# Kernel optimization log

Measured on AMD Instinct MI355X. Metric: run time of the kernel, lower is better.

## Reference

```python
import jax, jax.numpy as jnp
import numpy as np

# Dims fixed by ExpertC.__init__ defaults
INPUT_DIM, HIDDEN, OUT_DIM, NLAYERS = 1024, 256, 256, 2
D_STATE, EXPAND, HEADDIM = 32, 2, 32
D_INNER = EXPAND * HIDDEN                      # 512
NHEADS = D_INNER // HEADDIM                    # 16
CONV_DIM = D_INNER + 2 * D_STATE               # 576 (x, B, C; ngroups=1)
D_IN_PROJ = 2 * D_INNER + 2 * D_STATE + NHEADS # 1104 (z, xBC, dt)
KCONV = 4
B, L = 16, 2048
EPS = 1e-5


def setup_inputs() -> dict:
    key = jax.random.key(0)
    ks = iter(jax.random.split(key, 40))
    rn = lambda shape, s: jax.random.normal(next(ks), shape, jnp.float32) * s
    inp = {}
    inp["x"] = rn((B, L, INPUT_DIM), 1.0)
    inp["ip_w"] = rn((INPUT_DIM, HIDDEN), INPUT_DIM ** -0.5)
    inp["ip_b"] = jnp.zeros((HIDDEN,), jnp.float32)
    inp["m_inw"] = rn((NLAYERS, HIDDEN, D_IN_PROJ), HIDDEN ** -0.5)
    inp["m_inb"] = jnp.zeros((NLAYERS, D_IN_PROJ), jnp.float32)
    inp["m_convw"] = rn((NLAYERS, CONV_DIM, KCONV), 0.3)
    inp["m_convb"] = jnp.zeros((NLAYERS, CONV_DIM), jnp.float32)
    inp["m_dtb"] = rn((NLAYERS, NHEADS), 0.5)
    inp["m_Alog"] = jnp.log(1.0 + 15.0 * jax.random.uniform(next(ks), (NLAYERS, NHEADS), jnp.float32))
    inp["m_D"] = jnp.ones((NLAYERS, NHEADS), jnp.float32)
    inp["m_nw"] = jnp.ones((NLAYERS, D_INNER), jnp.float32)
    inp["m_outw"] = rn((NLAYERS, D_INNER, HIDDEN), D_INNER ** -0.5)
    inp["m_outb"] = jnp.zeros((NLAYERS, HIDDEN), jnp.float32)
    inp["rms_w"] = jnp.ones((NLAYERS, HIDDEN), jnp.float32)
    inp["ln1_w"] = jnp.ones((HIDDEN,), jnp.float32)
    inp["ln1_b"] = jnp.zeros((HIDDEN,), jnp.float32)
    inp["w1"] = rn((HIDDEN, 2 * HIDDEN), HIDDEN ** -0.5)
    inp["b1"] = jnp.zeros((2 * HIDDEN,), jnp.float32)
    inp["w2"] = rn((2 * HIDDEN, OUT_DIM), (2 * HIDDEN) ** -0.5)
    inp["b2"] = jnp.zeros((OUT_DIM,), jnp.float32)
    inp["ln2_w"] = jnp.ones((OUT_DIM,), jnp.float32)
    inp["ln2_b"] = jnp.zeros((OUT_DIM,), jnp.float32)
    return inp


def rmsnorm(x, w):
    return x * jax.lax.rsqrt(jnp.mean(x * x, axis=-1, keepdims=True) + EPS) * w


def layernorm(x, w, b):
    m = jnp.mean(x, axis=-1, keepdims=True)
    v = jnp.mean((x - m) ** 2, axis=-1, keepdims=True)
    return (x - m) * jax.lax.rsqrt(v + EPS) * w + b


def mamba_layer(x, inw, inb, convw, convb, dtb, Alog, D, nw, outw, outb):
    b, l, _ = x.shape
    zxbcdt = x @ inw + inb                                   # (b,l,1104)
    z, xBC, dt = jnp.split(zxbcdt, [D_INNER, D_INNER + CONV_DIM], axis=-1)
    dt = jax.nn.softplus(dt + dtb)                           # (b,l,h)
    # causal depthwise conv1d (kernel 4) + silu
    xp = jnp.pad(xBC, ((0, 0), (KCONV - 1, 0), (0, 0)))
    xBC = sum(xp[:, i:i + l, :] * convw[:, i] for i in range(KCONV)) + convb
    xBC = jax.nn.silu(xBC)
    xs, Bm, Cm = jnp.split(xBC, [D_INNER, D_INNER + D_STATE], axis=-1)
    xh = xs.reshape(b, l, NHEADS, HEADDIM)                   # (b,l,h,p)
    A = -jnp.exp(Alog)                                       # (h,)
    dA = jnp.exp(dt * A)                                     # (b,l,h)
    dtx = dt[..., None] * xh                                 # (b,l,h,p)

    def step(h, inp):
        dA_t, dtx_t, B_t, C_t = inp
        # h: (b,h,p,n)
        h = h * dA_t[:, :, None, None] + dtx_t[..., None] * B_t[:, None, None, :]
        y = jnp.einsum('bhpn,bn->bhp', h, C_t)
        return h, y

    h0 = jnp.zeros((b, NHEADS, HEADDIM, D_STATE), x.dtype)
    xs_t = (jnp.moveaxis(dA, 1, 0), jnp.moveaxis(dtx, 1, 0),
            jnp.moveaxis(Bm, 1, 0), jnp.moveaxis(Cm, 1, 0))
    _, ys = jax.lax.scan(step, h0, xs_t)                     # (l,b,h,p)
    y = jnp.moveaxis(ys, 0, 1) + D[None, None, :, None] * xh
    y = y.reshape(b, l, D_INNER)
    y = rmsnorm(y * jax.nn.silu(z), nw)                      # gated RMSNorm
    return y @ outw + outb


def _expert(x, ip_w, ip_b, m_inw, m_inb, m_convw, m_convb, m_dtb, m_Alog, m_D,
            m_nw, m_outw, m_outb, rms_w, ln1_w, ln1_b, w1, b1, w2, b2, ln2_w, ln2_b):
    if x.ndim == 2:
        x = x[:, None, :]
    x = x @ ip_w + ip_b
    for i in range(NLAYERS):
        res = x
        x = mamba_layer(x, m_inw[i], m_inb[i], m_convw[i], m_convb[i], m_dtb[i],
                        m_Alog[i], m_D[i], m_nw[i], m_outw[i], m_outb[i])
        x = rmsnorm(x + res, rms_w[i])
    x = layernorm(x, ln1_w, ln1_b)
    x = jax.nn.gelu(x @ w1 + b1, approximate=False)          # dropout is eval no-op
    x = x @ w2 + b2
    return layernorm(x, ln2_w, ln2_b)


def reference(x, ip_w, ip_b, m_inw, m_inb, m_convw, m_convb, m_dtb, m_Alog, m_D,
              m_nw, m_outw, m_outb, rms_w, ln1_w, ln1_b, w1, b1, w2, b2, ln2_w, ln2_b):
    return _expert(x, ip_w, ip_b, m_inw, m_inb, m_convw, m_convb, m_dtb, m_Alog, m_D,
                   m_nw, m_outw, m_outb, rms_w, ln1_w, ln1_b, w1, b1, w2, b2, ln2_w, ln2_b)
```

## Files before the change

### kernel.cpp

```cpp
#include <hip/hip_runtime.h>

typedef __bf16 bf16;
typedef __bf16 bf16x8 __attribute__((ext_vector_type(8)));
typedef float  f32x4  __attribute__((ext_vector_type(4)));

#define EPSF 1e-5f

__device__ __forceinline__ float bf2f(bf16 x) { return (float)x; }
__device__ __forceinline__ bf16  f2bf(float x) { return (bf16)x; }
__device__ __forceinline__ float siluf(float x) { return x / (1.f + expf(-x)); }

struct PrepackArgs {
    const float* W[7];
    bf16* TH[7];
    bf16* TL[7];
    int K[7];
    int N[7];
};

__global__ __launch_bounds__(256) void prepack_kernel(PrepackArgs a)
{
    int s = blockIdx.y;
    int idx = blockIdx.x * 256 + threadIdx.x;
    int K = a.K[s], N = a.N[s];
    if (idx >= K * N) return;
    int k = idx / N, n = idx - k * N;
    float v = a.W[s][idx];
    bf16 hi = f2bf(v);
    a.TH[s][(size_t)n * K + k] = hi;
    a.TL[s][(size_t)n * K + k] = f2bf(v - bf2f(hi));
}

__global__ __launch_bounds__(256) void gemm_hl(
    const bf16* __restrict__ AH, const bf16* __restrict__ AL,
    const float* __restrict__ Af, int lda,
    const bf16* __restrict__ WTh, const bf16* __restrict__ WTl,
    const float* __restrict__ bias,
    int N, int K,
    float* __restrict__ outF, int ldF,
    bf16* __restrict__ outB, int ldB,
    bf16* __restrict__ outH, bf16* __restrict__ outL, int ldH,
    int doGelu,
    const float* __restrict__ dtb, const float* __restrict__ Alog,
    float* __restrict__ dtf, float* __restrict__ dAf)
{
    __shared__ bf16 As [128][40];
    __shared__ bf16 Als[128][40];

    const int tid  = threadIdx.x;
    const int lane = tid & 63;
    const int wid  = tid >> 6;
    const int waveM = wid & 1, waveN = wid >> 1;
    const int m16 = lane & 15, quad = lane >> 4;
    const int row0 = blockIdx.x * 128;
    const int n0   = blockIdx.y * 64;

    f32x4 acc[4][2];
#pragma unroll
    for (int i = 0; i < 4; ++i)
#pragma unroll
        for (int j = 0; j < 2; ++j)
            acc[i][j] = (f32x4){0.f, 0.f, 0.f, 0.f};

    const int ar = tid >> 1, akc = (tid & 1) * 16;

    const int bn0 = min(n0 + waveN * 32 + m16,      N - 1);
    const int bn1 = min(n0 + waveN * 32 + 16 + m16, N - 1);
    const bf16* bH0p = WTh + (size_t)bn0 * K + quad * 8;
    const bf16* bH1p = WTh + (size_t)bn1 * K + quad * 8;
    const bf16* bL0p = WTl + (size_t)bn0 * K + quad * 8;
    const bf16* bL1p = WTl + (size_t)bn1 * K + quad * 8;

    bf16x8 bH[2], bL[2], bHn[2], bLn[2];
    bH[0] = *(const bf16x8*)(bH0p);
    bH[1] = *(const bf16x8*)(bH1p);
    bL[0] = *(const bf16x8*)(bL0p);
    bL[1] = *(const bf16x8*)(bL1p);

    for (int k0 = 0; k0 < K; k0 += 32) {
        if (AH) {
            const bf16* s0 = AH + (size_t)(row0 + ar) * lda + k0 + akc;
            const bf16* s1 = AL + (size_t)(row0 + ar) * lda + k0 + akc;
            *(uint4*)&As [ar][akc]     = *(const uint4*)s0;
            *(uint4*)&As [ar][akc + 8] = *(const uint4*)(s0 + 8);
            *(uint4*)&Als[ar][akc]     = *(const uint4*)s1;
            *(uint4*)&Als[ar][akc + 8] = *(const uint4*)(s1 + 8);
        } else {
            const float* asrc = Af + (size_t)(row0 + ar) * lda + k0 + akc;
            bf16* dh = &As [ar][akc];
            bf16* dl = &Als[ar][akc];
#pragma unroll
            for (int c = 0; c < 4; ++c) {
                float4 f = ((const float4*)asrc)[c];
#pragma unroll
                for (int e = 0; e < 4; ++e) {
                    float v = (&f.x)[e];
                    bf16 hi = f2bf(v);
                    dh[c * 4 + e] = hi;
                    dl[c * 4 + e] = f2bf(v - bf2f(hi));
                }
            }
        }
        __syncthreads();

        const bool more = (k0 + 32) < K;
        if (more) {
            int kn = k0 + 32;
            bHn[0] = *(const bf16x8*)(bH0p + kn);
            bHn[1] = *(const bf16x8*)(bH1p + kn);
            bLn[0] = *(const bf16x8*)(bL0p + kn);
            bLn[1] = *(const bf16x8*)(bL1p + kn);
        }

        bf16x8 aH[4], aL[4];
#pragma unroll
        for (int mi = 0; mi < 4; ++mi) {
            aH[mi] = *(const bf16x8*)&As [waveM * 64 + mi * 16 + m16][quad * 8];
            aL[mi] = *(const bf16x8*)&Als[waveM * 64 + mi * 16 + m16][quad * 8];
        }

#pragma unroll
        for (int mi = 0; mi < 4; ++mi)
#pragma unroll
            for (int ni = 0; ni < 2; ++ni) {
                acc[mi][ni] = __builtin_amdgcn_mfma_f32_16x16x32_bf16(
                    aH[mi], bH[ni], acc[mi][ni], 0, 0, 0);
                acc[mi][ni] = __builtin_amdgcn_mfma_f32_16x16x32_bf16(
                    aH[mi], bL[ni], acc[mi][ni], 0, 0, 0);
                acc[mi][ni] = __builtin_amdgcn_mfma_f32_16x16x32_bf16(
                    aL[mi], bH[ni], acc[mi][ni], 0, 0, 0);
            }
        __syncthreads();

        if (more) {
            bH[0] = bHn[0]; bH[1] = bHn[1];
            bL[0] = bLn[0]; bL[1] = bLn[1];
        }
    }

#pragma unroll
    for (int ni = 0; ni < 2; ++ni) {
        int col = n0 + waveN * 32 + ni * 16 + m16;
        if (col >= N) continue;
        float bv = bias ? bias[col] : 0.f;
#pragma unroll
        for (int mi = 0; mi < 4; ++mi) {
#pragma unroll
            for (int r = 0; r < 4; ++r) {
                int row = row0 + waveM * 64 + mi * 16 + quad * 4 + r;
                float v = acc[mi][ni][r] + bv;
                if (dtf && col >= 1088) {
                    int head = col - 1088;
                    float xx = v + dtb[head];
                    float sp = (xx > 20.f) ? xx : log1pf(expf(xx));
                    float A  = -expf(Alog[head]);
                    dtf[(size_t)row * 16 + head] = sp;
                    dAf[(size_t)row * 16 + head] = expf(sp * A);
                } else {
                    if (doGelu) v = 0.5f * v * (1.f + erff(v * 0.70710678118654752f));
                    if (outB) outB[(size_t)row * ldB + col] = f2bf(v);
                    if (outF) outF[(size_t)row * ldF + col] = v;
                    if (outH) {
                        bf16 hi = f2bf(v);
                        outH[(size_t)row * ldH + col] = hi;
                        outL[(size_t)row * ldH + col] = f2bf(v - bf2f(hi));
                    }
                }
            }
        }
    }
}

__global__ __launch_bounds__(192) void conv_kernel(
    const bf16* __restrict__ zx,
    const float* __restrict__ cw,
    const float* __restrict__ cb,
    float* __restrict__ xs,
    float* __restrict__ Bc,
    float* __restrict__ Cc)
{
    int row = blockIdx.x;
    int ch  = blockIdx.y * 192 + threadIdx.x;
    int l   = row & 2047;
    float acc = cb[ch];
#pragma unroll
    for (int i = 0; i < 4; ++i) {
        int ls = l + i - 3;
        if (ls >= 0)
            acc += bf2f(zx[(size_t)(row + i - 3) * 1104 + 512 + ch]) * cw[ch * 4 + i];
    }
    float s = siluf(acc);
    if (ch < 512)      xs[(size_t)row * 512 + ch]        = s;
    else if (ch < 544) Bc[(size_t)row * 32 + (ch - 512)] = s;
    else               Cc[(size_t)row * 32 + (ch - 544)] = s;
}

#define QCH   256
#define NCH   8

struct StepB  { float Bv[16]; float da, dtv, xv; };
struct StepBC { float Bv[16]; float Cv[16]; float da, dtv, xv; };

__device__ __forceinline__ void load_stepB(
    StepB& S, const float* Bc, const float* dtf, const float* dAf,
    const float* xs, size_t r, int h, int p, int nb)
{
    const float4* bp = (const float4*)(Bc + r * 32 + nb);
    *(float4*)&S.Bv[0]  = bp[0];
    *(float4*)&S.Bv[4]  = bp[1];
    *(float4*)&S.Bv[8]  = bp[2];
    *(float4*)&S.Bv[12] = bp[3];
    S.da  = dAf[r * 16 + h];
    S.dtv = dtf[r * 16 + h];
    S.xv  = xs[r * 512 + h * 32 + p];
}

__device__ __forceinline__ void load_stepBC(
    StepBC& S, const float* Bc, const float* Cc, const float* dtf,
    const float* dAf, const float* xs, size_t r, int h, int p, int nb)
{
    const float4* bp = (const float4*)(Bc + r * 32 + nb);
    *(float4*)&S.Bv[0]  = bp[0];
    *(float4*)&S.Bv[4]  = bp[1];
    *(float4*)&S.Bv[8]  = bp[2];
    *(float4*)&S.Bv[12] = bp[3];
    const float4* cp = (const float4*)(Cc + r * 32 + nb);
    *(float4*)&S.Cv[0]  = cp[0];
    *(float4*)&S.Cv[4]  = cp[1];
    *(float4*)&S.Cv[8]  = cp[2];
    *(float4*)&S.Cv[12] = cp[3];
    S.da  = dAf[r * 16 + h];
    S.dtv = dtf[r * 16 + h];
    S.xv  = xs[r * 512 + h * 32 + p];
}

__global__ __launch_bounds__(64) void scan_phase1(
    const float* __restrict__ xs,
    const float* __restrict__ Bc,
    const float* __restrict__ dtf,
    const float* __restrict__ dAf,
    float* __restrict__ cs,
    float* __restrict__ cp)
{
    int blk = blockIdx.x;
    int bh = blk >> 3, c = blk & (NCH - 1);
    int b = bh >> 4, h = bh & 15;
    int lane = threadIdx.x;
    int p = lane & 31, half = lane >> 5, nb = half * 16;
    float hs[16];
#pragma unroll
    for (int j = 0; j < 16; ++j) hs[j] = 0.f;
    float P = 1.f;
    size_t rb = (size_t)b * 2048 + (size_t)c * QCH;

    StepB S0, S1;
    load_stepB(S0, Bc, dtf, dAf, xs, rb, h, p, nb);

    for (int t = 0; t < QCH; t += 2) {
        load_stepB(S1, Bc, dtf, dAf, xs, rb + t + 1, h, p, nb);
        {
            float dtx = S0.dtv * S0.xv, da = S0.da;
#pragma unroll
            for (int j = 0; j < 16; ++j)
                hs[j] = fmaf(hs[j], da, dtx * S0.Bv[j]);
            P *= da;
        }
        if (t + 2 < QCH)
            load_stepB(S0, Bc, dtf, dAf, xs, rb + t + 2, h, p, nb);
        {
            float dtx = S1.dtv * S1.xv, da = S1.da;
#pragma unroll
            for (int j = 0; j < 16; ++j)
                hs[j] = fmaf(hs[j], da, dtx * S1.Bv[j]);
            P *= da;
        }
    }

    float* dst = cs + (size_t)blk * 1024 + lane * 16;
#pragma unroll
    for (int q = 0; q < 4; ++q)
        ((float4*)dst)[q] = (float4){hs[q*4], hs[q*4+1], hs[q*4+2], hs[q*4+3]};
    if (lane == 0) cp[blk] = P;
}

__global__ __launch_bounds__(64) void scan_phase2(
    float* __restrict__ cs,
    const float* __restrict__ cp)
{
    int bh = blockIdx.x;
    int lane = threadIdx.x;
    float H[16];
#pragma unroll
    for (int j = 0; j < 16; ++j) H[j] = 0.f;
    for (int c = 0; c < NCH; ++c) {
        float* base = cs + ((size_t)(bh * NCH + c)) * 1024 + lane * 16;
        float E[16];
#pragma unroll
        for (int q = 0; q < 4; ++q) {
            float4 v = ((const float4*)base)[q];
            E[q*4] = v.x; E[q*4+1] = v.y; E[q*4+2] = v.z; E[q*4+3] = v.w;
        }
        float P = cp[bh * NCH + c];
#pragma unroll
        for (int q = 0; q < 4; ++q)
            ((float4*)base)[q] = (float4){H[q*4], H[q*4+1], H[q*4+2], H[q*4+3]};
#pragma unroll
        for (int j = 0; j < 16; ++j)
            H[j] = fmaf(H[j], P, E[j]);
    }
}

__global__ __launch_bounds__(64) void scan_phase3(
    const float* __restrict__ xs,
    const float* __restrict__ Bc,
    const float* __restrict__ Cc,
    const float* __restrict__ dtf,
    const float* __restrict__ dAf,
    const float* __restrict__ Dv,
    const float* __restrict__ cs,
    bf16* __restrict__ y)
{
    int blk = blockIdx.x;
    int bh = blk >> 3, c = blk & (NCH - 1);
    int b = bh >> 4, h = bh & 15;
    int lane = threadIdx.x;
    int p = lane & 31, half = lane >> 5, nb = half * 16;
    float Dh = Dv[h];
    float hs[16];
    {
        const float* src = cs + (size_t)blk * 1024 + lane * 16;
#pragma unroll
        for (int q = 0; q < 4; ++q) {
            float4 v = ((const float4*)src)[q];
            hs[q*4] = v.x; hs[q*4+1] = v.y; hs[q*4+2] = v.z; hs[q*4+3] = v.w;
        }
    }
    size_t rb = (size_t)b * 2048 + (size_t)c * QCH;

    StepBC S0, S1;
    load_stepBC(S0, Bc, Cc, dtf, dAf, xs, rb, h, p, nb);

    for (int t = 0; t < QCH; t += 2) {
        load_stepBC(S1, Bc, Cc, dtf, dAf, xs, rb + t + 1, h, p, nb);
        {
            float dtx = S0.dtv * S0.xv, da = S0.da, yv = 0.f;
#pragma unroll
            for (int j = 0; j < 16; ++j) {
                hs[j] = fmaf(hs[j], da, dtx * S0.Bv[j]);
                yv = fmaf(hs[j], S0.Cv[j], yv);
            }
            yv += __shfl_xor(yv, 32);
            if (half == 0)
                y[(rb + t) * 512 + h * 32 + p] = f2bf(yv + Dh * S0.xv);
        }
        if (t + 2 < QCH)
            load_stepBC(S0, Bc, Cc, dtf, dAf, xs, rb + t + 2, h, p, nb);
        {
            float dtx = S1.dtv * S1.xv, da = S1.da, yv = 0.f;
#pragma unroll
            for (int j = 0; j < 16; ++j) {
                hs[j] = fmaf(hs[j], da, dtx * S1.Bv[j]);
                yv = fmaf(hs[j], S1.Cv[j], yv);
            }
            yv += __shfl_xor(yv, 32);
            if (half == 0)
                y[(rb + t + 1) * 512 + h * 32 + p] = f2bf(yv + Dh * S1.xv);
        }
    }
}

__global__ __launch_bounds__(64) void gaterms_kernel(
    const bf16* __restrict__ y,
    const bf16* __restrict__ zx,
    const float* __restrict__ nw,
    bf16* __restrict__ outH,
    bf16* __restrict__ outL)
{
    int row = blockIdx.x, lane = threadIdx.x;
    union { uint4 u; bf16 b[8]; } yv, zv, oh, ol;
    yv.u = *(const uint4*)(y  + (size_t)row * 512  + lane * 8);
    zv.u = *(const uint4*)(zx + (size_t)row * 1104 + lane * 8);
    float4 nv0 = *(const float4*)(nw + lane * 8);
    float4 nv1 = *(const float4*)(nw + lane * 8 + 4);
    float nvv[8] = {nv0.x, nv0.y, nv0.z, nv0.w, nv1.x, nv1.y, nv1.z, nv1.w};
    float g[8]; float ss = 0.f;
#pragma unroll
    for (int i = 0; i < 8; ++i) {
        float gate = siluf(bf2f(zv.b[i]));
        g[i] = bf2f(yv.b[i]) * gate;
        ss += g[i] * g[i];
    }
#pragma unroll
    for (int o = 1; o < 64; o <<= 1) ss += __shfl_xor(ss, o);
    float rms = rsqrtf(ss * (1.f / 512.f) + EPSF);
#pragma unroll
    for (int i = 0; i < 8; ++i) {
        float v = g[i] * rms * nvv[i];
        bf16 hi = f2bf(v);
        oh.b[i] = hi;
        ol.b[i] = f2bf(v - bf2f(hi));
    }
    *(uint4*)(outH + (size_t)row * 512 + lane * 8) = oh.u;
    *(uint4*)(outL + (size_t)row * 512 + lane * 8) = ol.u;
}

__global__ __launch_bounds__(64) void resrms_kernel(
    const float* __restrict__ mo,
    float* __restrict__ h,
    const float* __restrict__ w)
{
    int row = blockIdx.x, lane = threadIdx.x;
    float4 a = *(const float4*)(mo + (size_t)row * 256 + lane * 4);
    float4 r = *(const float4*)(h  + (size_t)row * 256 + lane * 4);
    float s0 = a.x + r.x, s1 = a.y + r.y, s2 = a.z + r.z, s3 = a.w + r.w;
    float ss = s0 * s0 + s1 * s1 + s2 * s2 + s3 * s3;
#pragma unroll
    for (int o = 1; o < 64; o <<= 1) ss += __shfl_xor(ss, o);
    float rms = rsqrtf(ss * (1.f / 256.f) + EPSF);
    float4 wv = *(const float4*)(w + lane * 4);
    *(float4*)(h + (size_t)row * 256 + lane * 4) =
        (float4){s0 * rms * wv.x, s1 * rms * wv.y, s2 * rms * wv.z, s3 * rms * wv.w};
}

__global__ __launch_bounds__(64) void ln_kernel(
    const float* __restrict__ x,
    const float* __restrict__ w,
    const float* __restrict__ b,
    bf16* __restrict__ outH,
    bf16* __restrict__ outL,
    float* __restrict__ outF)
{
    int row = blockIdx.x, lane = threadIdx.x;
    float4 v = *(const float4*)(x + (size_t)row * 256 + lane * 4);
    float sum = v.x + v.y + v.z + v.w;
    float sq  = v.x * v.x + v.y * v.y + v.z * v.z + v.w * v.w;
#pragma unroll
    for (int o = 1; o < 64; o <<= 1) { sum += __shfl_xor(sum, o); sq += __shfl_xor(sq, o); }
    float m  = sum * (1.f / 256.f);
    float var = sq * (1.f / 256.f) - m * m;
    float is = rsqrtf(var + EPSF);
    float4 wv = *(const float4*)(w + lane * 4);
    float4 bv = *(const float4*)(b + lane * 4);
    float o0 = (v.x - m) * is * wv.x + bv.x;
    float o1 = (v.y - m) * is * wv.y + bv.y;
    float o2 = (v.z - m) * is * wv.z + bv.z;
    float o3 = (v.w - m) * is * wv.w + bv.w;
    if (outH) {
        union { uint2 u; bf16 bb[4]; } oh, ol;
        float o[4] = {o0, o1, o2, o3};
#pragma unroll
        for (int i = 0; i < 4; ++i) {
            bf16 hi = f2bf(o[i]);
            oh.bb[i] = hi;
            ol.bb[i] = f2bf(o[i] - bf2f(hi));
        }
        *(uint2*)(outH + (size_t)row * 256 + lane * 4) = oh.u;
        *(uint2*)(outL + (size_t)row * 256 + lane * 4) = ol.u;
    }
    if (outF)
        *(float4*)(outF + (size_t)row * 256 + lane * 4) = (float4){o0, o1, o2, o3};
}

extern "C" void kernel_launch(void* const* d_in, const int* in_sizes, int n_in,
                              void* d_out, int out_size, void* d_ws, size_t ws_size,
                              hipStream_t stream)
{
    const float* x      = (const float*)d_in[0];
    const float* ip_w   = (const float*)d_in[1];
    const float* ip_b   = (const float*)d_in[2];
    const float* m_inw  = (const float*)d_in[3];
    const float* m_inb  = (const float*)d_in[4];
    const float* m_convw= (const float*)d_in[5];
    const float* m_convb= (const float*)d_in[6];
    const float* m_dtb  = (const float*)d_in[7];
    const float* m_Alog = (const float*)d_in[8];
    const float* m_D    = (const float*)d_in[9];
    const float* m_nw   = (const float*)d_in[10];
    const float* m_outw = (const float*)d_in[11];
    const float* m_outb = (const float*)d_in[12];
    const float* rms_w  = (const float*)d_in[13];
    const float* ln1_w  = (const float*)d_in[14];
    const float* ln1_b  = (const float*)d_in[15];
    const float* w1     = (const float*)d_in[16];
    const float* b1     = (const float*)d_in[17];
    const float* w2     = (const float*)d_in[18];
    const float* b2     = (const float*)d_in[19];
    const float* ln2_w  = (const float*)d_in[20];
    const float* ln2_b  = (const float*)d_in[21];

    const int M = 32768;
    char* wsb = (char*)d_ws;
    size_t off = 0;
    auto alloc = [&](size_t bytes) {
        void* p = wsb + off;
        off += (bytes + 255) & ~(size_t)255;
        return p;
    };
    bf16*  zx   = (bf16*) alloc((size_t)M * 1104 * 2);
    float* h    = (float*)alloc((size_t)M * 256 * 4);
    float* U1   = (float*)alloc((size_t)M * 512 * 4);
    float* Bc   = (float*)alloc((size_t)M * 32 * 4);
    float* Cc   = (float*)alloc((size_t)M * 32 * 4);
    float* dtf  = (float*)alloc((size_t)M * 16 * 4);
    float* dAf  = (float*)alloc((size_t)M * 16 * 4);
    bf16*  ybuf = (bf16*) alloc((size_t)M * 512 * 2);
    float* cs   = (float*)alloc((size_t)2048 * 1024 * 4);
    float* cpb  = (float*)alloc((size_t)2048 * 4);
    bf16* ipTH   = (bf16*)alloc(262144 * 2);
    bf16* ipTL   = (bf16*)alloc(262144 * 2);
    bf16* inwTH0 = (bf16*)alloc(282624 * 2);
    bf16* inwTL0 = (bf16*)alloc(282624 * 2);
    bf16* inwTH1 = (bf16*)alloc(282624 * 2);
    bf16* inwTL1 = (bf16*)alloc(282624 * 2);
    bf16* outwTH0= (bf16*)alloc(131072 * 2);
    bf16* outwTL0= (bf16*)alloc(131072 * 2);
    bf16* outwTH1= (bf16*)alloc(131072 * 2);
    bf16* outwTL1= (bf16*)alloc(131072 * 2);
    bf16* w1TH   = (bf16*)alloc(131072 * 2);
    bf16* w1TL   = (bf16*)alloc(131072 * 2);
    bf16* w2TH   = (bf16*)alloc(131072 * 2);
    bf16* w2TL   = (bf16*)alloc(131072 * 2);
    (void)ws_size; (void)in_sizes; (void)n_in; (void)out_size;

    float* xs      = U1;
    bf16*  normedH = (bf16*)U1;
    bf16*  normedL = normedH + (size_t)M * 512;
    bf16*  tbH     = (bf16*)U1;
    bf16*  tbL     = tbH + (size_t)M * 256;
    float* mo      = (float*)zx;
    bf16*  gH      = (bf16*)zx;
    bf16*  gL      = gH + (size_t)M * 512;
    float* ubuf    = (float*)ybuf;

    PrepackArgs pa;
    pa.W[0] = ip_w;               pa.TH[0] = ipTH;    pa.TL[0] = ipTL;    pa.K[0] = 1024; pa.N[0] = 256;
    pa.W[1] = m_inw;              pa.TH[1] = inwTH0;  pa.TL[1] = inwTL0;  pa.K[1] = 256;  pa.N[1] = 1104;
    pa.W[2] = m_inw + 256*1104;   pa.TH[2] = inwTH1;  pa.TL[2] = inwTL1;  pa.K[2] = 256;  pa.N[2] = 1104;
    pa.W[3] = m_outw;             pa.TH[3] = outwTH0; pa.TL[3] = outwTL0; pa.K[3] = 512;  pa.N[3] = 256;
    pa.W[4] = m_outw + 512*256;   pa.TH[4] = outwTH1; pa.TL[4] = outwTL1; pa.K[4] = 512;  pa.N[4] = 256;
    pa.W[5] = w1;                 pa.TH[5] = w1TH;    pa.TL[5] = w1TL;    pa.K[5] = 256;  pa.N[5] = 512;
    pa.W[6] = w2;                 pa.TH[6] = w2TH;    pa.TL[6] = w2TL;    pa.K[6] = 512;  pa.N[6] = 256;
    prepack_kernel<<<dim3(1104, 7), 256, 0, stream>>>(pa);

    dim3 blk(256);

    gemm_hl<<<dim3(256, 4), blk, 0, stream>>>(
        nullptr, nullptr, x, 1024, ipTH, ipTL, ip_b, 256, 1024,
        h, 256, nullptr, 0, nullptr, nullptr, 0, 0,
        nullptr, nullptr, nullptr, nullptr);

    for (int L = 0; L < 2; ++L) {
        const bf16* inwTH = L ? inwTH1 : inwTH0;
        const bf16* inwTL = L ? inwTL1 : inwTL0;
        const bf16* outwTH= L ? outwTH1 : outwTH0;
        const bf16* outwTL= L ? outwTL1 : outwTL0;
        const float* inb = m_inb  + (size_t)L * 1104;
        const float* cw  = m_convw+ (size_t)L * 576 * 4;
        const float* cb  = m_convb+ (size_t)L * 576;
        const float* dtb = m_dtb  + L * 16;
        const float* Al  = m_Alog + L * 16;
        const float* Dv  = m_D    + L * 16;
        const float* nw  = m_nw   + (size_t)L * 512;
        const float* ob  = m_outb + (size_t)L * 256;
        const float* rw  = rms_w  + (size_t)L * 256;

        gemm_hl<<<dim3(256, 18), blk, 0, stream>>>(
            nullptr, nullptr, h, 256, inwTH, inwTL, inb, 1104, 256,
            nullptr, 0, zx, 1104, nullptr, nullptr, 0, 0,
            dtb, Al, dtf, dAf);
        conv_kernel<<<dim3(M, 3), 192, 0, stream>>>(zx, cw, cb, xs, Bc, Cc);
        scan_phase1<<<2048, 64, 0, stream>>>(xs, Bc, dtf, dAf, cs, cpb);
        scan_phase2<<<256, 64, 0, stream>>>(cs, cpb);
        scan_phase3<<<2048, 64, 0, stream>>>(xs, Bc, Cc, dtf, dAf, Dv, cs, ybuf);
        gaterms_kernel<<<M, 64, 0, stream>>>(ybuf, zx, nw, normedH, normedL);
        gemm_hl<<<dim3(256, 4), blk, 0, stream>>>(
            normedH, normedL, nullptr, 512, outwTH, outwTL, ob, 256, 512,
            mo, 256, nullptr, 0, nullptr, nullptr, 0, 0,
            nullptr, nullptr, nullptr, nullptr);
        resrms_kernel<<<M, 64, 0, stream>>>(mo, h, rw);
    }

    ln_kernel<<<M, 64, 0, stream>>>(h, ln1_w, ln1_b, tbH, tbL, nullptr);
    gemm_hl<<<dim3(256, 8), blk, 0, stream>>>(
        tbH, tbL, nullptr, 256, w1TH, w1TL, b1, 512, 256,
        nullptr, 0, nullptr, 0, gH, gL, 512, 1,
        nullptr, nullptr, nullptr, nullptr);
    gemm_hl<<<dim3(256, 4), blk, 0, stream>>>(
        gH, gL, nullptr, 512, w2TH, w2TL, b2, 256, 512,
        ubuf, 256, nullptr, 0, nullptr, nullptr, 0, 0,
        nullptr, nullptr, nullptr, nullptr);
    ln_kernel<<<M, 64, 0, stream>>>(ubuf, ln2_w, ln2_b, nullptr, nullptr, (float*)d_out);
}
```

Before: 1.523 ms.

## Vectorize conv, shorten scan chunks, pack rows per block, prepack hi/lo activations

Several independent changes land together. The conv kernel now handles 8 channels per thread with vector loads and stores, and the scan uses 32 chunks of 64 steps instead of 8 of 256, with four waves per block and split y accumulators. Scan output is written into the x slot of zx, which drops the separate y buffer, and resrms/ip GEMM emit bf16 hi/lo copies so the in_proj GEMM skips the fp32 split. Row kernels pack four rows per 256-thread block; this trades launch count and serial scan depth for a larger chunk-state buffer and more phase-2 work.

New measurement: 1.564 ms. 1.03x slower.

```diff
diff --git a/kernel.cpp b/kernel.cpp
--- a/kernel.cpp
+++ b/kernel.cpp
@@ -87,19 +87,22 @@
             *(uint4*)&Als[ar][akc + 8] = *(const uint4*)(s1 + 8);
         } else {
             const float* asrc = Af + (size_t)(row0 + ar) * lda + k0 + akc;
-            bf16* dh = &As [ar][akc];
-            bf16* dl = &Als[ar][akc];
-#pragma unroll
-            for (int c = 0; c < 4; ++c) {
-                float4 f = ((const float4*)asrc)[c];
-#pragma unroll
-                for (int e = 0; e < 4; ++e) {
-                    float v = (&f.x)[e];
-                    bf16 hi = f2bf(v);
-                    dh[c * 4 + e] = hi;
-                    dl[c * 4 + e] = f2bf(v - bf2f(hi));
-                }
+            float f[16];
+            *(float4*)&f[0]  = ((const float4*)asrc)[0];
+            *(float4*)&f[4]  = ((const float4*)asrc)[1];
+            *(float4*)&f[8]  = ((const float4*)asrc)[2];
+            *(float4*)&f[12] = ((const float4*)asrc)[3];
+            bf16 hv[16], lv[16];
+#pragma unroll
+            for (int c = 0; c < 16; ++c) {
+                bf16 hi = f2bf(f[c]);
+                hv[c] = hi;
+                lv[c] = f2bf(f[c] - bf2f(hi));
             }
+            *(uint4*)&As [ar][akc]     = *(uint4*)&hv[0];
+            *(uint4*)&As [ar][akc + 8] = *(uint4*)&hv[8];
+            *(uint4*)&Als[ar][akc]     = *(uint4*)&lv[0];
+            *(uint4*)&Als[ar][akc + 8] = *(uint4*)&lv[8];
         }
         __syncthreads();
 
@@ -171,32 +174,66 @@
     }
 }
 
-__global__ __launch_bounds__(192) void conv_kernel(
+__global__ __launch_bounds__(256) void conv_kernel(
     const bf16* __restrict__ zx,
     const float* __restrict__ cw,
-    const float* __restrict__ cb,
+    const float* __restrict__ cbias,
     float* __restrict__ xs,
     float* __restrict__ Bc,
     float* __restrict__ Cc)
 {
-    int row = blockIdx.x;
-    int ch  = blockIdx.y * 192 + threadIdx.x;
+    int g = blockIdx.x * 256 + threadIdx.x;
+    if (g >= 32768 * 72) return;
+    int row = g / 72;
+    int cb8 = g - row * 72;
+    int ch  = cb8 * 8;
     int l   = row & 2047;
-    float acc = cb[ch];
+
+    float4 wv[8];
+#pragma unroll
+    for (int c = 0; c < 8; ++c)
+        wv[c] = *(const float4*)(cw + (ch + c) * 4);
+
+    float acc[8];
+    {
+        float4 b0 = *(const float4*)(cbias + ch);
+        float4 b1 = *(const float4*)(cbias + ch + 4);
+        acc[0] = b0.x; acc[1] = b0.y; acc[2] = b0.z; acc[3] = b0.w;
+        acc[4] = b1.x; acc[5] = b1.y; acc[6] = b1.z; acc[7] = b1.w;
+    }
+
 #pragma unroll
     for (int i = 0; i < 4; ++i) {
         int ls = l + i - 3;
-        if (ls >= 0)
-            acc += bf2f(zx[(size_t)(row + i - 3) * 1104 + 512 + ch]) * cw[ch * 4 + i];
-    }
-    float s = siluf(acc);
-    if (ch < 512)      xs[(size_t)row * 512 + ch]        = s;
-    else if (ch < 544) Bc[(size_t)row * 32 + (ch - 512)] = s;
-    else               Cc[(size_t)row * 32 + (ch - 544)] = s;
-}
-
-#define QCH   256
-#define NCH   8
+        if (ls >= 0) {
+            bf16x8 v = *(const bf16x8*)(zx + (size_t)(row + i - 3) * 1104 + 512 + ch);
+#pragma unroll
+            for (int c = 0; c < 8; ++c)
+                acc[c] = fmaf(bf2f(v[c]), (&wv[c].x)[i], acc[c]);
+        }
+    }
+
+    float s[8];
+#pragma unroll
+    for (int c = 0; c < 8; ++c) s[c] = siluf(acc[c]);
+
+    if (cb8 < 64) {
+        float* dst = xs + (size_t)row * 512 + ch;
+        ((float4*)dst)[0] = (float4){s[0], s[1], s[2], s[3]};
+        ((float4*)dst)[1] = (float4){s[4], s[5], s[6], s[7]};
+    } else if (cb8 < 68) {
+        float* dst = Bc + (size_t)row * 32 + (ch - 512);
+        ((float4*)dst)[0] = (float4){s[0], s[1], s[2], s[3]};
+        ((float4*)dst)[1] = (float4){s[4], s[5], s[6], s[7]};
+    } else {
+        float* dst = Cc + (size_t)row * 32 + (ch - 544);
+        ((float4*)dst)[0] = (float4){s[0], s[1], s[2], s[3]};
+        ((float4*)dst)[1] = (float4){s[4], s[5], s[6], s[7]};
+    }
+}
+
+#define QCH   64
+#define NCH   32
 
 struct StepB  { float Bv[16]; float da, dtv, xv; };
 struct StepBC { float Bv[16]; float Cv[16]; float da, dtv, xv; };
@@ -234,7 +271,7 @@
     S.xv  = xs[r * 512 + h * 32 + p];
 }
 
-__global__ __launch_bounds__(64) void scan_phase1(
+__global__ __launch_bounds__(256) void scan_phase1(
     const float* __restrict__ xs,
     const float* __restrict__ Bc,
     const float* __restrict__ dtf,
@@ -242,10 +279,10 @@
     float* __restrict__ cs,
     float* __restrict__ cp)
 {
-    int blk = blockIdx.x;
-    int bh = blk >> 3, c = blk & (NCH - 1);
+    int blk = blockIdx.x * 4 + (threadIdx.x >> 6);
+    int bh = blk >> 5, c = blk & (NCH - 1);
     int b = bh >> 4, h = bh & 15;
-    int lane = threadIdx.x;
+    int lane = threadIdx.x & 63;
     int p = lane & 31, half = lane >> 5, nb = half * 16;
     float hs[16];
 #pragma unroll
@@ -310,7 +347,7 @@
     }
 }
 
-__global__ __launch_bounds__(64) void scan_phase3(
+__global__ __launch_bounds__(256) void scan_phase3(
     const float* __restrict__ xs,
     const float* __restrict__ Bc,
     const float* __restrict__ Cc,
@@ -318,12 +355,12 @@
     const float* __restrict__ dAf,
     const float* __restrict__ Dv,
     const float* __restrict__ cs,
-    bf16* __restrict__ y)
-{
-    int blk = blockIdx.x;
-    int bh = blk >> 3, c = blk & (NCH - 1);
+    bf16* __restrict__ zx)
+{
+    int blk = blockIdx.x * 4 + (threadIdx.x >> 6);
+    int bh = blk >> 5, c = blk & (NCH - 1);
     int b = bh >> 4, h = bh & 15;
-    int lane = threadIdx.x;
+    int lane = threadIdx.x & 63;
     int p = lane & 31, half = lane >> 5, nb = half * 16;
     float Dh = Dv[h];
     float hs[16];
@@ -343,42 +380,50 @@
     for (int t = 0; t < QCH; t += 2) {
         load_stepBC(S1, Bc, Cc, dtf, dAf, xs, rb + t + 1, h, p, nb);
         {
-            float dtx = S0.dtv * S0.xv, da = S0.da, yv = 0.f;
-#pragma unroll
-            for (int j = 0; j < 16; ++j) {
-                hs[j] = fmaf(hs[j], da, dtx * S0.Bv[j]);
-                yv = fmaf(hs[j], S0.Cv[j], yv);
+            float dtx = S0.dtv * S0.xv, da = S0.da;
+            float y0 = 0.f, y1 = 0.f, y2 = 0.f, y3 = 0.f;
+#pragma unroll
+            for (int j = 0; j < 16; j += 4) {
+                hs[j]   = fmaf(hs[j],   da, dtx * S0.Bv[j]);   y0 = fmaf(hs[j],   S0.Cv[j],   y0);
+                hs[j+1] = fmaf(hs[j+1], da, dtx * S0.Bv[j+1]); y1 = fmaf(hs[j+1], S0.Cv[j+1], y1);
+                hs[j+2] = fmaf(hs[j+2], da, dtx * S0.Bv[j+2]); y2 = fmaf(hs[j+2], S0.Cv[j+2], y2);
+                hs[j+3] = fmaf(hs[j+3], da, dtx * S0.Bv[j+3]); y3 = fmaf(hs[j+3], S0.Cv[j+3], y3);
             }
+            float yv = (y0 + y1) + (y2 + y3);
             yv += __shfl_xor(yv, 32);
             if (half == 0)
-                y[(rb + t) * 512 + h * 32 + p] = f2bf(yv + Dh * S0.xv);
+                zx[(rb + t) * 1104 + 512 + h * 32 + p] = f2bf(yv + Dh * S0.xv);
         }
         if (t + 2 < QCH)
             load_stepBC(S0, Bc, Cc, dtf, dAf, xs, rb + t + 2, h, p, nb);
         {
-            float dtx = S1.dtv * S1.xv, da = S1.da, yv = 0.f;
-#pragma unroll
-            for (int j = 0; j < 16; ++j) {
-                hs[j] = fmaf(hs[j], da, dtx * S1.Bv[j]);
-                yv = fmaf(hs[j], S1.Cv[j], yv);
+            float dtx = S1.dtv * S1.xv, da = S1.da;
+            float y0 = 0.f, y1 = 0.f, y2 = 0.f, y3 = 0.f;
+#pragma unroll
+            for (int j = 0; j < 16; j += 4) {
+                hs[j]   = fmaf(hs[j],   da, dtx * S1.Bv[j]);   y0 = fmaf(hs[j],   S1.Cv[j],   y0);
+                hs[j+1] = fmaf(hs[j+1], da, dtx * S1.Bv[j+1]); y1 = fmaf(hs[j+1], S1.Cv[j+1], y1);
+                hs[j+2] = fmaf(hs[j+2], da, dtx * S1.Bv[j+2]); y2 = fmaf(hs[j+2], S1.Cv[j+2], y2);
+                hs[j+3] = fmaf(hs[j+3], da, dtx * S1.Bv[j+3]); y3 = fmaf(hs[j+3], S1.Cv[j+3], y3);
             }
+            float yv = (y0 + y1) + (y2 + y3);
             yv += __shfl_xor(yv, 32);
             if (half == 0)
-                y[(rb + t + 1) * 512 + h * 32 + p] = f2bf(yv + Dh * S1.xv);
-        }
-    }
-}
-
-__global__ __launch_bounds__(64) void gaterms_kernel(
-    const bf16* __restrict__ y,
+                zx[(rb + t + 1) * 1104 + 512 + h * 32 + p] = f2bf(yv + Dh * S1.xv);
+        }
+    }
+}
+
+__global__ __launch_bounds__(256) void gaterms_kernel(
     const bf16* __restrict__ zx,
     const float* __restrict__ nw,
     bf16* __restrict__ outH,
     bf16* __restrict__ outL)
 {
-    int row = blockIdx.x, lane = threadIdx.x;
+    int row = blockIdx.x * 4 + (threadIdx.x >> 6);
+    int lane = threadIdx.x & 63;
     union { uint4 u; bf16 b[8]; } yv, zv, oh, ol;
-    yv.u = *(const uint4*)(y  + (size_t)row * 512  + lane * 8);
+    yv.u = *(const uint4*)(zx + (size_t)row * 1104 + 512 + lane * 8);
     zv.u = *(const uint4*)(zx + (size_t)row * 1104 + lane * 8);
     float4 nv0 = *(const float4*)(nw + lane * 8);
     float4 nv1 = *(const float4*)(nw + lane * 8 + 4);
@@ -404,12 +449,15 @@
     *(uint4*)(outL + (size_t)row * 512 + lane * 8) = ol.u;
 }
 
-__global__ __launch_bounds__(64) void resrms_kernel(
+__global__ __launch_bounds__(256) void resrms_kernel(
     const float* __restrict__ mo,
     float* __restrict__ h,
-    const float* __restrict__ w)
-{
-    int row = blockIdx.x, lane = threadIdx.x;
+    const float* __restrict__ w,
+    bf16* __restrict__ oH,
+    bf16* __restrict__ oL)
+{
+    int row = blockIdx.x * 4 + (threadIdx.x >> 6);
+    int lane = threadIdx.x & 63;
     float4 a = *(const float4*)(mo + (size_t)row * 256 + lane * 4);
     float4 r = *(const float4*)(h  + (size_t)row * 256 + lane * 4);
     float s0 = a.x + r.x, s1 = a.y + r.y, s2 = a.z + r.z, s3 = a.w + r.w;
@@ -418,11 +466,22 @@
     for (int o = 1; o < 64; o <<= 1) ss += __shfl_xor(ss, o);
     float rms = rsqrtf(ss * (1.f / 256.f) + EPSF);
     float4 wv = *(const float4*)(w + lane * 4);
-    *(float4*)(h + (size_t)row * 256 + lane * 4) =
-        (float4){s0 * rms * wv.x, s1 * rms * wv.y, s2 * rms * wv.z, s3 * rms * wv.w};
-}
-
-__global__ __launch_bounds__(64) void ln_kernel(
+    float o0 = s0 * rms * wv.x, o1 = s1 * rms * wv.y;
+    float o2 = s2 * rms * wv.z, o3 = s3 * rms * wv.w;
+    *(float4*)(h + (size_t)row * 256 + lane * 4) = (float4){o0, o1, o2, o3};
+    union { uint2 u; bf16 bb[4]; } uh, ul;
+    float o[4] = {o0, o1, o2, o3};
+#pragma unroll
+    for (int i = 0; i < 4; ++i) {
+        bf16 hi = f2bf(o[i]);
+        uh.bb[i] = hi;
+        ul.bb[i] = f2bf(o[i] - bf2f(hi));
+    }
+    *(uint2*)(oH + (size_t)row * 256 + lane * 4) = uh.u;
+    *(uint2*)(oL + (size_t)row * 256 + lane * 4) = ul.u;
+}
+
+__global__ __launch_bounds__(256) void ln_kernel(
     const float* __restrict__ x,
     const float* __restrict__ w,
     const float* __restrict__ b,
@@ -430,7 +489,8 @@
     bf16* __restrict__ outL,
     float* __restrict__ outF)
 {
-    int row = blockIdx.x, lane = threadIdx.x;
+    int row = blockIdx.x * 4 + (threadIdx.x >> 6);
+    int lane = threadIdx.x & 63;
     float4 v = *(const float4*)(x + (size_t)row * 256 + lane * 4);
     float sum = v.x + v.y + v.z + v.w;
     float sq  = v.x * v.x + v.y * v.y + v.z * v.z + v.w * v.w;
@@ -503,9 +563,8 @@
     float* Cc   = (float*)alloc((size_t)M * 32 * 4);
     float* dtf  = (float*)alloc((size_t)M * 16 * 4);
     float* dAf  = (float*)alloc((size_t)M * 16 * 4);
-    bf16*  ybuf = (bf16*) alloc((size_t)M * 512 * 2);
-    float* cs   = (float*)alloc((size_t)2048 * 1024 * 4);
-    float* cpb  = (float*)alloc((size_t)2048 * 4);
+    float* cs   = (float*)alloc((size_t)8192 * 1024 * 4);
+    float* cpb  = (float*)alloc((size_t)8192 * 4);
     bf16* ipTH   = (bf16*)alloc(262144 * 2);
     bf16* ipTL   = (bf16*)alloc(262144 * 2);
     bf16* inwTH0 = (bf16*)alloc(282624 * 2);
@@ -523,6 +582,8 @@
     (void)ws_size; (void)in_sizes; (void)n_in; (void)out_size;
 
     float* xs      = U1;
+    bf16*  hH      = (bf16*)U1;
+    bf16*  hL      = hH + (size_t)M * 256;
     bf16*  normedH = (bf16*)U1;
     bf16*  normedL = normedH + (size_t)M * 512;
     bf16*  tbH     = (bf16*)U1;
@@ -530,7 +591,7 @@
     float* mo      = (float*)zx;
     bf16*  gH      = (bf16*)zx;
     bf16*  gL      = gH + (size_t)M * 512;
-    float* ubuf    = (float*)ybuf;
+    float* ubuf    = (float*)cs;
 
     PrepackArgs pa;
     pa.W[0] = ip_w;               pa.TH[0] = ipTH;    pa.TL[0] = ipTL;    pa.K[0] = 1024; pa.N[0] = 256;
@@ -546,7 +607,7 @@
 
     gemm_hl<<<dim3(256, 4), blk, 0, stream>>>(
         nullptr, nullptr, x, 1024, ipTH, ipTL, ip_b, 256, 1024,
-        h, 256, nullptr, 0, nullptr, nullptr, 0, 0,
+        h, 256, nullptr, 0, hH, hL, 256, 0,
         nullptr, nullptr, nullptr, nullptr);
 
     for (int L = 0; L < 2; ++L) {
@@ -565,22 +626,22 @@
         const float* rw  = rms_w  + (size_t)L * 256;
 
         gemm_hl<<<dim3(256, 18), blk, 0, stream>>>(
-            nullptr, nullptr, h, 256, inwTH, inwTL, inb, 1104, 256,
+            hH, hL, nullptr, 256, inwTH, inwTL, inb, 1104, 256,
             nullptr, 0, zx, 1104, nullptr, nullptr, 0, 0,
             dtb, Al, dtf, dAf);
-        conv_kernel<<<dim3(M, 3), 192, 0, stream>>>(zx, cw, cb, xs, Bc, Cc);
-        scan_phase1<<<2048, 64, 0, stream>>>(xs, Bc, dtf, dAf, cs, cpb);
+        conv_kernel<<<9216, 256, 0, stream>>>(zx, cw, cb, xs, Bc, Cc);
+        scan_phase1<<<2048, 256, 0, stream>>>(xs, Bc, dtf, dAf, cs, cpb);
         scan_phase2<<<256, 64, 0, stream>>>(cs, cpb);
-        scan_phase3<<<2048, 64, 0, stream>>>(xs, Bc, Cc, dtf, dAf, Dv, cs, ybuf);
-        gaterms_kernel<<<M, 64, 0, stream>>>(ybuf, zx, nw, normedH, normedL);
+        scan_phase3<<<2048, 256, 0, stream>>>(xs, Bc, Cc, dtf, dAf, Dv, cs, zx);
+        gaterms_kernel<<<M / 4, 256, 0, stream>>>(zx, nw, normedH, normedL);
         gemm_hl<<<dim3(256, 4), blk, 0, stream>>>(
             normedH, normedL, nullptr, 512, outwTH, outwTL, ob, 256, 512,
             mo, 256, nullptr, 0, nullptr, nullptr, 0, 0,
             nullptr, nullptr, nullptr, nullptr);
-        resrms_kernel<<<M, 64, 0, stream>>>(mo, h, rw);
-    }
-
-    ln_kernel<<<M, 64, 0, stream>>>(h, ln1_w, ln1_b, tbH, tbL, nullptr);
+        resrms_kernel<<<M / 4, 256, 0, stream>>>(mo, h, rw, hH, hL);
+    }
+
+    ln_kernel<<<M / 4, 256, 0, stream>>>(h, ln1_w, ln1_b, tbH, tbL, nullptr);
     gemm_hl<<<dim3(256, 8), blk, 0, stream>>>(
         tbH, tbL, nullptr, 256, w1TH, w1TL, b1, 512, 256,
         nullptr, 0, nullptr, 0, gH, gL, 512, 1,
@@ -589,5 +650,5 @@
         gH, gL, nullptr, 512, w2TH, w2TL, b2, 256, 512,
         ubuf, 256, nullptr, 0, nullptr, nullptr, 0, 0,
         nullptr, nullptr, nullptr, nullptr);
-    ln_kernel<<<M, 64, 0, stream>>>(ubuf, ln2_w, ln2_b, nullptr, nullptr, (float*)d_out);
-}
+    ln_kernel<<<M / 4, 256, 0, stream>>>(ubuf, ln2_w, ln2_b, nullptr, nullptr, (float*)d_out);
+}
```
